# Kernel tuning notes

Measured on AMD Instinct MI355X. Metric: run time of the kernel, lower is better.

## Reference

```python
import jax, jax.numpy as jnp
import numpy as np

DIM = 1024
NUM_HEADS = 16
HEAD_DIM = DIM // NUM_HEADS
EPS = 1e-6


def _xavier(key, shape, gain=0.1):
    fan_in, fan_out = shape[1], shape[0]
    limit = gain * np.sqrt(6.0 / (fan_in + fan_out))
    return jax.random.uniform(key, shape, jnp.float32, -limit, limit)


def setup_inputs() -> dict:
    key = jax.random.key(0)
    kx, kq, kk, kv, ko = jax.random.split(key, 5)
    B, N = 4, 4096
    return {
        "x": jax.random.normal(kx, (B, N, DIM), jnp.float32),
        "Wq": _xavier(kq, (DIM, DIM)), "bq": jnp.zeros((DIM,), jnp.float32),
        "Wk": _xavier(kk, (DIM, DIM)), "bk": jnp.zeros((DIM,), jnp.float32),
        "Wv": _xavier(kv, (DIM, DIM)), "bv": jnp.zeros((DIM,), jnp.float32),
        "Wo": _xavier(ko, (DIM, DIM)), "bo": jnp.zeros((DIM,), jnp.float32),
    }


def _phi(x):
    # ELU feature map: elu(x) + 1 ensures non-negativity
    return jax.nn.elu(x) + 1.0


def reference(x, Wq, bq, Wk, bk, Wv, bv, Wo, bo):
    B, N, D = x.shape
    H, Hd = NUM_HEADS, HEAD_DIM
    # torch Linear: y = x @ W.T + b
    Q = (x @ Wq.T + bq).reshape(B, N, H, Hd).transpose(0, 2, 1, 3)
    K = (x @ Wk.T + bk).reshape(B, N, H, Hd).transpose(0, 2, 1, 3)
    V = (x @ Wv.T + bv).reshape(B, N, H, Hd).transpose(0, 2, 1, 3)
    Q = _phi(Q)
    K = _phi(K)
    KV = jnp.einsum('bhnd,bhne->bhde', K, V)          # [B,H,Hd,Hd] state
    out = jnp.einsum('bhnd,bhde->bhne', Q, KV)        # [B,H,N,Hd]
    Z = K.sum(axis=2)                                  # [B,H,Hd]
    norm = jnp.einsum('bhnd,bhd->bhn', Q, Z)[..., None] + EPS
    out = out / norm
    out = out.transpose(0, 2, 1, 3).reshape(B, N, D)
    return out @ Wo.T + bo
```

## Files before the change

kernel.cpp:

```cpp
#include <hip/hip_runtime.h>
#include <math.h>

#define DIMC 1024
#define SEQ 4096
#define BATCH 4
#define NH 16
#define HD 64
#define MTOT (BATCH * SEQ)
#define NSPLIT 8
#define PELEMS (64 * 64 * 64 + 64 * 64)
#define EPS 1e-6f
#define NKT (DIMC / 64)

typedef __bf16 bf16x8 __attribute__((ext_vector_type(8)));
typedef __bf16 bf16x4 __attribute__((ext_vector_type(4)));
typedef __bf16 bf16x2 __attribute__((ext_vector_type(2)));
typedef float  f32x4  __attribute__((ext_vector_type(4)));

#define MFMA16 __builtin_amdgcn_mfma_f32_16x16x32_bf16

__device__ __forceinline__ float phi_f(float x) {
    return x > 0.0f ? x + 1.0f : __expf(x);
}

__global__ __launch_bounds__(256) void cvt_all(
    const float* __restrict__ x,
    const float* __restrict__ Wq, const float* __restrict__ Wk,
    const float* __restrict__ Wv, const float* __restrict__ Wo,
    __bf16* __restrict__ xb,
    __bf16* __restrict__ Wqb, __bf16* __restrict__ Wkb,
    __bf16* __restrict__ Wvb, __bf16* __restrict__ Wob)
{
    const size_t big = (size_t)MTOT * DIMC;
    const size_t wsz = (size_t)DIMC * DIMC;
    size_t i = ((size_t)blockIdx.x * 256 + threadIdx.x) * 4;
    const float* src; __bf16* dst; size_t off;
    if (i < big) { src = x; dst = xb; off = i; }
    else {
        size_t j = i - big;
        int w = (int)(j >> 20);
        off = j & (wsz - 1);
        switch (w) {
            case 0: src = Wq; dst = Wqb; break;
            case 1: src = Wk; dst = Wkb; break;
            case 2: src = Wv; dst = Wvb; break;
            default: src = Wo; dst = Wob; break;
        }
    }
    float4 v = *(const float4*)(src + off);
    bf16x4 o = { (__bf16)v.x, (__bf16)v.y, (__bf16)v.z, (__bf16)v.w };
    *(bf16x4*)(dst + off) = o;
}

template<int OUT_BF16>
__device__ __forceinline__ void gemm_tile256(
    const __bf16* __restrict__ X, const __bf16* __restrict__ W,
    const float* __restrict__ bias, void* __restrict__ Yv,
    int m0, int n0, int do_phi)
{
    __shared__ __attribute__((aligned(16))) __bf16 lds[65536];
    const int tid  = threadIdx.x;
    const int wave = tid >> 6, lane = tid & 63;
    const int wm = wave >> 2, wn = wave & 3;
    const int fr = lane & 15, fkb = lane >> 4;
    const int fsw = fr & 7;
    const int srow = lane >> 3;
    const int sblk = (lane & 7) ^ srow;

    const __bf16* Asrc = X + (size_t)(m0 + wave * 8 + srow) * DIMC + sblk * 8;
    const __bf16* Bsrc = W + (size_t)(n0 + wave * 8 + srow) * DIMC + sblk * 8;
    __bf16* lw = lds + wave * 512;

    auto stage = [&](int isB, int h, int tt, int bb) {
        const __bf16* s = (isB ? Bsrc : Asrc)
                          + (size_t)(h * 128) * DIMC + (size_t)tt * 64;
        __bf16* d = lw + bb * 32768 + isB * 16384 + h * 8192;
        #pragma unroll
        for (int g = 0; g < 2; ++g)
            __builtin_amdgcn_global_load_lds(
                (const __attribute__((address_space(1))) void*)(s + (size_t)g * 64 * DIMC),
                (__attribute__((address_space(3))) void*)(d + g * 4096),
                16, 0, 0);
    };
    auto lda = [&](int bb, int i, int ks) -> bf16x8 {
        return *(const bf16x8*)(lds + bb * 32768 + wm * 8192
                 + (i * 16 + fr) * 64 + (((ks * 4 + fkb) ^ fsw) * 8));
    };
    auto ldb = [&](int bb, int j, int ks) -> bf16x8 {
        return *(const bf16x8*)(lds + bb * 32768 + 16384 + (wn >> 1) * 8192
                 + ((wn & 1) * 64 + j * 16 + fr) * 64 + (((ks * 4 + fkb) ^ fsw) * 8));
    };

    f32x4 acc[8][4] = {};
    bf16x8 a[4][2], b[4][2];

    stage(1, 0, 0, 0); stage(1, 1, 0, 0); stage(0, 0, 0, 0); stage(0, 1, 0, 0);
    stage(1, 0, 1, 1); stage(1, 1, 1, 1); stage(0, 0, 1, 1);
    asm volatile("s_waitcnt vmcnt(6)" ::: "memory");
    __builtin_amdgcn_s_barrier();

    #pragma unroll 2
    for (int t = 0; t < NKT; ++t) {
        const int buf = t & 1;
        #pragma unroll
        for (int i = 0; i < 4; ++i)
            #pragma unroll
            for (int ks = 0; ks < 2; ++ks) a[i][ks] = lda(buf, i, ks);
        #pragma unroll
        for (int j = 0; j < 2; ++j)
            #pragma unroll
            for (int ks = 0; ks < 2; ++ks) b[j][ks] = ldb(buf, j, ks);
        if (t + 1 < NKT) stage(0, 1, t + 1, buf ^ 1);
        __builtin_amdgcn_s_barrier();
        asm volatile("s_waitcnt lgkmcnt(0)" ::: "memory");
        __builtin_amdgcn_s_setprio(1);
        #pragma unroll
        for (int i = 0; i < 4; ++i)
            #pragma unroll
            for (int j = 0; j < 2; ++j)
                #pragma unroll
                for (int ks = 0; ks < 2; ++ks)
                    acc[i][j] = MFMA16(a[i][ks], b[j][ks], acc[i][j], 0, 0, 0);
        __builtin_amdgcn_s_setprio(0);
        __builtin_amdgcn_s_barrier();
        #pragma unroll
        for (int j = 2; j < 4; ++j)
            #pragma unroll
            for (int ks = 0; ks < 2; ++ks) b[j][ks] = ldb(buf, j, ks);
        __builtin_amdgcn_s_barrier();
        asm volatile("s_waitcnt lgkmcnt(0)" ::: "memory");
        __builtin_amdgcn_s_setprio(1);
        #pragma unroll
        for (int i = 0; i < 4; ++i)
            #pragma unroll
            for (int j = 2; j < 4; ++j)
                #pragma unroll
                for (int ks = 0; ks < 2; ++ks)
                    acc[i][j] = MFMA16(a[i][ks], b[j][ks], acc[i][j], 0, 0, 0);
        __builtin_amdgcn_s_setprio(0);
        __builtin_amdgcn_s_barrier();
        #pragma unroll
        for (int i = 0; i < 4; ++i)
            #pragma unroll
            for (int ks = 0; ks < 2; ++ks) a[i][ks] = lda(buf, i + 4, ks);
        if (t + 2 < NKT) stage(1, 0, t + 2, buf);
        __builtin_amdgcn_s_barrier();
        asm volatile("s_waitcnt lgkmcnt(0)" ::: "memory");
        __builtin_amdgcn_s_setprio(1);
        #pragma unroll
        for (int i = 0; i < 4; ++i)
            #pragma unroll
            for (int j = 2; j < 4; ++j)
                #pragma unroll
                for (int ks = 0; ks < 2; ++ks)
                    acc[i + 4][j] = MFMA16(a[i][ks], b[j][ks], acc[i + 4][j], 0, 0, 0);
        __builtin_amdgcn_s_setprio(0);
        __builtin_amdgcn_s_barrier();
        if (t + 2 < NKT) { stage(1, 1, t + 2, buf); stage(0, 0, t + 2, buf); }
        __builtin_amdgcn_s_setprio(1);
        #pragma unroll
        for (int i = 0; i < 4; ++i)
            #pragma unroll
            for (int j = 0; j < 2; ++j)
                #pragma unroll
                for (int ks = 0; ks < 2; ++ks)
                    acc[i + 4][j] = MFMA16(a[i][ks], b[j][ks], acc[i + 4][j], 0, 0, 0);
        __builtin_amdgcn_s_setprio(0);
        if (t < NKT - 2)       asm volatile("s_waitcnt vmcnt(6)" ::: "memory");
        else if (t == NKT - 2) asm volatile("s_waitcnt vmcnt(0)" ::: "memory");
        __builtin_amdgcn_s_barrier();
    }

    const int col_l = lane & 15, quad = lane >> 4;
    #pragma unroll
    for (int j = 0; j < 4; ++j) {
        const int gcol = n0 + wn * 64 + j * 16 + col_l;
        const float bb = bias[gcol];
        #pragma unroll
        for (int i = 0; i < 8; ++i) {
            #pragma unroll
            for (int r = 0; r < 4; ++r) {
                const int grow = m0 + wm * 128 + i * 16 + quad * 4 + r;
                float v = acc[i][j][r] + bb;
                if (do_phi) v = phi_f(v);
                if (OUT_BF16)
                    ((__bf16*)Yv)[(size_t)grow * DIMC + gcol] = (__bf16)v;
                else
                    ((float*)Yv)[(size_t)grow * DIMC + gcol] = v;
            }
        }
    }
}

__global__ __launch_bounds__(512, 2) void gemm_qkv(
    const __bf16* __restrict__ X,
    const __bf16* __restrict__ Wq, const __bf16* __restrict__ Wk,
    const __bf16* __restrict__ Wv,
    const float* __restrict__ bq, const float* __restrict__ bk,
    const float* __restrict__ bv,
    __bf16* __restrict__ Q, __bf16* __restrict__ K, __bf16* __restrict__ V)
{
    const int l = blockIdx.x;
    const int xcd = l & 7, s = l >> 3;
    const int mat = s >> 5;
    const int t = s & 31;
    const int nb = t & 3;
    const int m_idx = xcd * 8 + (t >> 2);
    const __bf16* W = (mat == 0) ? Wq : (mat == 1) ? Wk : Wv;
    const float* bias = (mat == 0) ? bq : (mat == 1) ? bk : bv;
    __bf16* Y = (mat == 0) ? Q : (mat == 1) ? K : V;
    gemm_tile256<1>(X, W, bias, Y, m_idx * 256, nb * 256, mat != 2);
}

__global__ __launch_bounds__(512, 2) void gemm_out(
    const __bf16* __restrict__ A, const __bf16* __restrict__ Wo,
    const float* __restrict__ bo, float* __restrict__ out)
{
    const int l = blockIdx.x;
    const int xcd = l & 7, s = l >> 3;
    const int m_idx = xcd * 8 + (s >> 2);
    const int nb = s & 3;
    gemm_tile256<0>(A, Wo, bo, out, m_idx * 256, nb * 256, 0);
}

__global__ __launch_bounds__(256) void kv_z_kernel(
    const __bf16* __restrict__ Kb, const __bf16* __restrict__ Vb,
    float* __restrict__ P)
{
    __shared__ __attribute__((aligned(16))) __bf16 Kt[64 * 36];
    __shared__ __attribute__((aligned(16))) __bf16 Vt[64 * 36];
    __shared__ float zs[64];
    const int tid = threadIdx.x, wave = tid >> 6, lane = tid & 63;
    const int bh = blockIdx.x, b = bh >> 4, h = bh & 15;
    const int split = blockIdx.y;
    const int n0 = split * (SEQ / NSPLIT);
    const int dg = (tid & 15) * 4;
    const int u2 = (tid >> 4) * 2;
    const int fr = lane & 15, fk = (lane >> 4) * 8;
    const __bf16* Kp = Kb + ((size_t)b * SEQ + n0) * DIMC + h * HD;
    const __bf16* Vp = Vb + ((size_t)b * SEQ + n0) * DIMC + h * HD;

    if (tid < 64) zs[tid] = 0.0f;
    f32x4 acc[4] = {};
    float zp[4] = {};

    for (int c = 0; c < SEQ / NSPLIT; c += 32) {
        bf16x4 ka = *(const bf16x4*)(Kp + (size_t)(c + u2) * DIMC + dg);
        bf16x4 kb = *(const bf16x4*)(Kp + (size_t)(c + u2 + 1) * DIMC + dg);
        bf16x4 va = *(const bf16x4*)(Vp + (size_t)(c + u2) * DIMC + dg);
        bf16x4 vb = *(const bf16x4*)(Vp + (size_t)(c + u2 + 1) * DIMC + dg);
        __syncthreads();
        #pragma unroll
        for (int q = 0; q < 4; ++q) {
            zp[q] += (float)ka[q] + (float)kb[q];
            *(bf16x2*)(Kt + (dg + q) * 36 + u2) = bf16x2{ka[q], kb[q]};
            *(bf16x2*)(Vt + (dg + q) * 36 + u2) = bf16x2{va[q], vb[q]};
        }
        __syncthreads();

        const __bf16* ar = Kt + (wave * 16 + fr) * 36 + fk;
        bf16x4 alo = *(const bf16x4*)ar, ahi = *(const bf16x4*)(ar + 4);
        bf16x8 af = {alo[0],alo[1],alo[2],alo[3],ahi[0],ahi[1],ahi[2],ahi[3]};
        #pragma unroll
        for (int j = 0; j < 4; ++j) {
            const __bf16* br = Vt + (j * 16 + fr) * 36 + fk;
            bf16x4 blo = *(const bf16x4*)br, bhi = *(const bf16x4*)(br + 4);
            bf16x8 bf = {blo[0],blo[1],blo[2],blo[3],bhi[0],bhi[1],bhi[2],bhi[3]};
            acc[j] = __builtin_amdgcn_mfma_f32_16x16x32_bf16(af, bf, acc[j], 0, 0, 0);
        }
    }

    #pragma unroll
    for (int q = 0; q < 4; ++q) atomicAdd(&zs[dg + q], zp[q]);
    __syncthreads();

    float* KVp = P + (size_t)split * PELEMS + bh * 4096;
    const int col_l = lane & 15, quad = lane >> 4;
    #pragma unroll
    for (int j = 0; j < 4; ++j)
        #pragma unroll
        for (int r = 0; r < 4; ++r)
            KVp[(wave * 16 + quad * 4 + r) * 64 + j * 16 + col_l] = acc[j][r];
    if (tid < 64)
        P[(size_t)split * PELEMS + 64 * 64 * 64 + bh * 64 + tid] = zs[tid];
}

__global__ __launch_bounds__(256) void reduce_partials(
    const float* __restrict__ P, float* __restrict__ F)
{
    const int i = blockIdx.x * 256 + threadIdx.x;
    if (i < PELEMS) {
        float s = 0.0f;
        #pragma unroll
        for (int sp = 0; sp < NSPLIT; ++sp) s += P[(size_t)sp * PELEMS + i];
        F[i] = s;
    }
}

__global__ __launch_bounds__(256) void attn_apply(
    const __bf16* __restrict__ Qb, const float* __restrict__ KV,
    const float* __restrict__ Z, __bf16* __restrict__ Ab)
{
    __shared__ __align__(16) float KVs[64][64];
    __shared__ __align__(16) float Qs[32][64];
    __shared__ float Zs[64];
    __shared__ float rnorm[32];
    const int tid = threadIdx.x;
    const int bh = blockIdx.y;
    const int b = bh >> 4, h = bh & 15;
    const int n0 = blockIdx.x * 32;

    const float* KVp = KV + (size_t)bh * HD * HD;
    #pragma unroll
    for (int r = 0; r < 4; ++r) {
        const int idx = (r * 256 + tid) * 4;
        *(float4*)&((float*)KVs)[idx] = *(const float4*)(KVp + idx);
    }
    const __bf16* Qp = Qb + ((size_t)(b * SEQ + n0)) * DIMC + h * HD;
    {
        const int tok = tid >> 3, col = (tid & 7) * 8;
        bf16x8 q8 = *(const bf16x8*)(Qp + (size_t)tok * DIMC + col);
        #pragma unroll
        for (int q = 0; q < 8; ++q) Qs[tok][col + q] = (float)q8[q];
    }
    if (tid < 64) Zs[tid] = Z[bh * HD + tid];
    __syncthreads();

    if (tid < 32) {
        float s = 0.0f;
        #pragma unroll
        for (int d = 0; d < 64; ++d) s += Qs[tid][d] * Zs[d];
        rnorm[tid] = 1.0f / (s + EPS);
    }
    __syncthreads();

    const int trow = tid >> 3;
    const int e0 = (tid & 7) * 8;
    float out[8] = {};
    #pragma unroll
    for (int d = 0; d < 64; ++d) {
        const float q = Qs[trow][d];
        #pragma unroll
        for (int j = 0; j < 8; ++j) out[j] = fmaf(q, KVs[d][e0 + j], out[j]);
    }
    const float rn = rnorm[trow];
    __bf16* Op = Ab + ((size_t)(b * SEQ + n0 + trow)) * DIMC + h * HD + e0;
    bf16x8 o;
    #pragma unroll
    for (int j = 0; j < 8; ++j) o[j] = (__bf16)(out[j] * rn);
    *(bf16x8*)Op = o;
}

extern "C" void kernel_launch(void* const* d_in, const int* in_sizes, int n_in,
                              void* d_out, int out_size, void* d_ws, size_t ws_size,
                              hipStream_t stream) {
    const float* x  = (const float*)d_in[0];
    const float* Wq = (const float*)d_in[1];
    const float* bq = (const float*)d_in[2];
    const float* Wk = (const float*)d_in[3];
    const float* bk = (const float*)d_in[4];
    const float* Wv = (const float*)d_in[5];
    const float* bv = (const float*)d_in[6];
    const float* Wo = (const float*)d_in[7];
    const float* bo = (const float*)d_in[8];
    float* out = (float*)d_out;

    const size_t big = (size_t)MTOT * DIMC;
    const size_t wsz = (size_t)DIMC * DIMC;
    __bf16* wsp = (__bf16*)d_ws;
    __bf16* xb  = wsp;
    __bf16* Wqb = xb + big;
    __bf16* Wkb = Wqb + wsz;
    __bf16* Wvb = Wkb + wsz;
    __bf16* Wob = Wvb + wsz;
    __bf16* Qb  = Wob + wsz;
    __bf16* Kb  = Qb + big;
    __bf16* Vb  = Kb + big;
    __bf16* Ab  = xb;
    float*  P   = (float*)(Vb + big);
    float*  F   = P + (size_t)NSPLIT * PELEMS;
    float*  KV  = F;
    float*  Z   = F + 64 * 64 * 64;

    const size_t ntot = big + 4 * wsz;
    cvt_all<<<dim3((int)(ntot / 1024)), 256, 0, stream>>>(
        x, Wq, Wk, Wv, Wo, xb, Wqb, Wkb, Wvb, Wob);

    gemm_qkv<<<dim3(768), 512, 0, stream>>>(
        xb, Wqb, Wkb, Wvb, bq, bk, bv, Qb, Kb, Vb);

    kv_z_kernel<<<dim3(BATCH * NH, NSPLIT), 256, 0, stream>>>(Kb, Vb, P);
    reduce_partials<<<dim3((PELEMS + 255) / 256), 256, 0, stream>>>(P, F);
    attn_apply<<<dim3(SEQ / 32, BATCH * NH), 256, 0, stream>>>(Qb, KV, Z, Ab);

    gemm_out<<<dim3(256), 512, 0, stream>>>(Ab, Wob, bo, out);
}
```

Baseline: 370.7 us.

## Fuse Q/K/V GEMMs into one persistent block looping over three weight matrices

The QKV projection now launches 256 blocks instead of 768. Each block computes the same 256x256 output tile for Wq, Wk and Wv in turn, running one continuous 48-step K pipeline. The epilogue fires every 16 steps, writes that matrix's output and clears the accumulators, so the double-buffered prefetch runs across matrix boundaries without draining. This removes per-block prologue and tail cost and reuses the X tile's cache locality. The cost is fewer blocks, which can hurt load balance and occupancy across the CUs, and extra branching in the loop.

```diff
diff --git a/kernel.cpp b/kernel.cpp
--- a/kernel.cpp
+++ b/kernel.cpp
@@ -10,7 +10,6 @@
 #define NSPLIT 8
 #define PELEMS (64 * 64 * 64 + 64 * 64)
 #define EPS 1e-6f
-#define NKT (DIMC / 64)
 
 typedef __bf16 bf16x8 __attribute__((ext_vector_type(8)));
 typedef __bf16 bf16x4 __attribute__((ext_vector_type(4)));
@@ -52,12 +51,17 @@
     *(bf16x4*)(dst + off) = o;
 }
 
-template<int OUT_BF16>
-__device__ __forceinline__ void gemm_tile256(
-    const __bf16* __restrict__ X, const __bf16* __restrict__ W,
-    const float* __restrict__ bias, void* __restrict__ Yv,
-    int m0, int n0, int do_phi)
-{
+template<int NMAT, int OUT_BF16>
+__device__ __forceinline__ void gemm_persist(
+    const __bf16* __restrict__ X,
+    const __bf16* __restrict__ W0, const __bf16* __restrict__ W1,
+    const __bf16* __restrict__ W2,
+    const float* __restrict__ bias0, const float* __restrict__ bias1,
+    const float* __restrict__ bias2,
+    void* __restrict__ Y0, void* __restrict__ Y1, void* __restrict__ Y2,
+    int m0, int n0)
+{
+    constexpr int TNKT = NMAT * 16;
     __shared__ __attribute__((aligned(16))) __bf16 lds[65536];
     const int tid  = threadIdx.x;
     const int wave = tid >> 6, lane = tid & 63;
@@ -67,13 +71,21 @@
     const int srow = lane >> 3;
     const int sblk = (lane & 7) ^ srow;
 
-    const __bf16* Asrc = X + (size_t)(m0 + wave * 8 + srow) * DIMC + sblk * 8;
-    const __bf16* Bsrc = W + (size_t)(n0 + wave * 8 + srow) * DIMC + sblk * 8;
+    const size_t aoff = (size_t)(m0 + wave * 8 + srow) * DIMC + sblk * 8;
+    const size_t boff = (size_t)(n0 + wave * 8 + srow) * DIMC + sblk * 8;
+    const __bf16* Asrc = X + aoff;
+    const __bf16* Bs0 = W0 + boff;
+    const __bf16* Bs1 = W1 + boff;
+    const __bf16* Bs2 = W2 + boff;
     __bf16* lw = lds + wave * 512;
 
-    auto stage = [&](int isB, int h, int tt, int bb) {
-        const __bf16* s = (isB ? Bsrc : Asrc)
-                          + (size_t)(h * 128) * DIMC + (size_t)tt * 64;
+    auto bsel = [&](int t) -> const __bf16* {
+        if (NMAT == 1) return Bs0;
+        const int mat = t >> 4;
+        return mat == 0 ? Bs0 : (mat == 1 ? Bs1 : Bs2);
+    };
+    auto stage = [&](const __bf16* base, int h, int kblk, int isB, int bb) {
+        const __bf16* s = base + (size_t)(h * 128) * DIMC + (size_t)kblk * 64;
         __bf16* d = lw + bb * 32768 + isB * 16384 + h * 8192;
         #pragma unroll
         for (int g = 0; g < 2; ++g)
@@ -94,13 +106,15 @@
     f32x4 acc[8][4] = {};
     bf16x8 a[4][2], b[4][2];
 
-    stage(1, 0, 0, 0); stage(1, 1, 0, 0); stage(0, 0, 0, 0); stage(0, 1, 0, 0);
-    stage(1, 0, 1, 1); stage(1, 1, 1, 1); stage(0, 0, 1, 1);
+    stage(Bs0, 0, 0, 1, 0); stage(Bs0, 1, 0, 1, 0);
+    stage(Asrc, 0, 0, 0, 0); stage(Asrc, 1, 0, 0, 0);
+    stage(Bs0, 0, 1, 1, 1); stage(Bs0, 1, 1, 1, 1);
+    stage(Asrc, 0, 1, 0, 1);
     asm volatile("s_waitcnt vmcnt(6)" ::: "memory");
     __builtin_amdgcn_s_barrier();
 
     #pragma unroll 2
-    for (int t = 0; t < NKT; ++t) {
+    for (int t = 0; t < TNKT; ++t) {
         const int buf = t & 1;
         #pragma unroll
         for (int i = 0; i < 4; ++i)
@@ -110,7 +124,7 @@
         for (int j = 0; j < 2; ++j)
             #pragma unroll
             for (int ks = 0; ks < 2; ++ks) b[j][ks] = ldb(buf, j, ks);
-        if (t + 1 < NKT) stage(0, 1, t + 1, buf ^ 1);
+        if (t + 1 < TNKT) stage(Asrc, 1, (t + 1) & 15, 0, buf ^ 1);
         __builtin_amdgcn_s_barrier();
         asm volatile("s_waitcnt lgkmcnt(0)" ::: "memory");
         __builtin_amdgcn_s_setprio(1);
@@ -143,7 +157,7 @@
         for (int i = 0; i < 4; ++i)
             #pragma unroll
             for (int ks = 0; ks < 2; ++ks) a[i][ks] = lda(buf, i + 4, ks);
-        if (t + 2 < NKT) stage(1, 0, t + 2, buf);
+        if (t + 2 < TNKT) stage(bsel(t + 2), 0, (t + 2) & 15, 1, buf);
         __builtin_amdgcn_s_barrier();
         asm volatile("s_waitcnt lgkmcnt(0)" ::: "memory");
         __builtin_amdgcn_s_setprio(1);
@@ -156,7 +170,10 @@
                     acc[i + 4][j] = MFMA16(a[i][ks], b[j][ks], acc[i + 4][j], 0, 0, 0);
         __builtin_amdgcn_s_setprio(0);
         __builtin_amdgcn_s_barrier();
-        if (t + 2 < NKT) { stage(1, 1, t + 2, buf); stage(0, 0, t + 2, buf); }
+        if (t + 2 < TNKT) {
+            stage(bsel(t + 2), 1, (t + 2) & 15, 1, buf);
+            stage(Asrc, 0, (t + 2) & 15, 0, buf);
+        }
         __builtin_amdgcn_s_setprio(1);
         #pragma unroll
         for (int i = 0; i < 4; ++i)
@@ -166,27 +183,35 @@
                 for (int ks = 0; ks < 2; ++ks)
                     acc[i + 4][j] = MFMA16(a[i][ks], b[j][ks], acc[i + 4][j], 0, 0, 0);
         __builtin_amdgcn_s_setprio(0);
-        if (t < NKT - 2)       asm volatile("s_waitcnt vmcnt(6)" ::: "memory");
-        else if (t == NKT - 2) asm volatile("s_waitcnt vmcnt(0)" ::: "memory");
-        __builtin_amdgcn_s_barrier();
-    }
-
-    const int col_l = lane & 15, quad = lane >> 4;
-    #pragma unroll
-    for (int j = 0; j < 4; ++j) {
-        const int gcol = n0 + wn * 64 + j * 16 + col_l;
-        const float bb = bias[gcol];
-        #pragma unroll
-        for (int i = 0; i < 8; ++i) {
-            #pragma unroll
-            for (int r = 0; r < 4; ++r) {
-                const int grow = m0 + wm * 128 + i * 16 + quad * 4 + r;
-                float v = acc[i][j][r] + bb;
-                if (do_phi) v = phi_f(v);
-                if (OUT_BF16)
-                    ((__bf16*)Yv)[(size_t)grow * DIMC + gcol] = (__bf16)v;
-                else
-                    ((float*)Yv)[(size_t)grow * DIMC + gcol] = v;
+        if (t < TNKT - 2)       asm volatile("s_waitcnt vmcnt(6)" ::: "memory");
+        else if (t == TNKT - 2) asm volatile("s_waitcnt vmcnt(0)" ::: "memory");
+        __builtin_amdgcn_s_barrier();
+
+        if ((t & 15) == 15) {
+            const int mat = (NMAT == 1) ? 0 : (t >> 4);
+            const float* bias = (mat == 0) ? bias0 : (mat == 1) ? bias1 : bias2;
+            void* Yv = (mat == 0) ? Y0 : (mat == 1) ? Y1 : Y2;
+            const int col_l = lane & 15, quad = lane >> 4;
+            const int cbase = n0 + wn * 64 + col_l;
+            float bb[4];
+            #pragma unroll
+            for (int j = 0; j < 4; ++j) bb[j] = bias[cbase + j * 16];
+            #pragma unroll
+            for (int i = 0; i < 8; ++i) {
+                #pragma unroll
+                for (int r = 0; r < 4; ++r) {
+                    const size_t grow = (size_t)(m0 + wm * 128 + i * 16 + quad * 4 + r) * DIMC;
+                    #pragma unroll
+                    for (int j = 0; j < 4; ++j) {
+                        float v = acc[i][j][r] + bb[j];
+                        if (NMAT == 3 && mat != 2) v = phi_f(v);
+                        if (OUT_BF16)
+                            ((__bf16*)Yv)[grow + cbase + j * 16] = (__bf16)v;
+                        else
+                            ((float*)Yv)[grow + cbase + j * 16] = v;
+                        acc[i][j][r] = 0.0f;
+                    }
+                }
             }
         }
     }
@@ -202,14 +227,10 @@
 {
     const int l = blockIdx.x;
     const int xcd = l & 7, s = l >> 3;
-    const int mat = s >> 5;
-    const int t = s & 31;
-    const int nb = t & 3;
-    const int m_idx = xcd * 8 + (t >> 2);
-    const __bf16* W = (mat == 0) ? Wq : (mat == 1) ? Wk : Wv;
-    const float* bias = (mat == 0) ? bq : (mat == 1) ? bk : bv;
-    __bf16* Y = (mat == 0) ? Q : (mat == 1) ? K : V;
-    gemm_tile256<1>(X, W, bias, Y, m_idx * 256, nb * 256, mat != 2);
+    const int m_idx = xcd * 8 + (s >> 2);
+    const int nb = s & 3;
+    gemm_persist<3, 1>(X, Wq, Wk, Wv, bq, bk, bv,
+                       (void*)Q, (void*)K, (void*)V, m_idx * 256, nb * 256);
 }
 
 __global__ __launch_bounds__(512, 2) void gemm_out(
@@ -220,7 +241,9 @@
     const int xcd = l & 7, s = l >> 3;
     const int m_idx = xcd * 8 + (s >> 2);
     const int nb = s & 3;
-    gemm_tile256<0>(A, Wo, bo, out, m_idx * 256, nb * 256, 0);
+    gemm_persist<1, 0>(A, Wo, Wo, Wo, bo, bo, bo,
+                       (void*)out, (void*)out, (void*)out,
+                       m_idx * 256, nb * 256);
 }
 
 __global__ __launch_bounds__(256) void kv_z_kernel(
@@ -386,7 +409,7 @@
     cvt_all<<<dim3((int)(ntot / 1024)), 256, 0, stream>>>(
         x, Wq, Wk, Wv, Wo, xb, Wqb, Wkb, Wvb, Wob);
 
-    gemm_qkv<<<dim3(768), 512, 0, stream>>>(
+    gemm_qkv<<<dim3(256), 512, 0, stream>>>(
         xb, Wqb, Wkb, Wvb, bq, bk, bv, Qb, Kb, Vb);
 
     kv_z_kernel<<<dim3(BATCH * NH, NSPLIT), 256, 0, stream>>>(Kb, Vb, P);
```

Measured after the change: 370.9 us. Within noise of the previous version (+0.1%).
